# Kernel optimization log

Measured on AMD Instinct MI355X. Metric: run time of the kernel, lower is better.

## Reference

```python
import jax, jax.numpy as jnp
import numpy as np

BIT_DEPTH = 8  # feature squeezing

def setup_inputs() -> dict:
    key = jax.random.key(0)
    ks = jax.random.split(key, 8)
    B, C, H, W = 8, 256, 64, 64
    Cq = C // 8
    x = jax.random.normal(ks[0], (B, C, H, W), dtype=jnp.float32)
    # 1x1 conv weights stored as [out, in] (kernel dims squeezed)
    wq = jax.random.normal(ks[1], (Cq, C), dtype=jnp.float32) * 0.05
    bq = jax.random.normal(ks[2], (Cq,), dtype=jnp.float32) * 0.05
    wk = jax.random.normal(ks[3], (Cq, C), dtype=jnp.float32) * 0.05
    bk = jax.random.normal(ks[4], (Cq,), dtype=jnp.float32) * 0.05
    wv = jax.random.normal(ks[5], (C, C), dtype=jnp.float32) * 0.05
    bv = jax.random.normal(ks[6], (C,), dtype=jnp.float32) * 0.05
    gamma = jax.random.normal(ks[7], (1,), dtype=jnp.float32) * 0.1
    return {"x": x, "wq": wq, "bq": bq, "wk": wk, "bk": bk, "wv": wv, "bv": bv, "gamma": gamma}

def reference(x, wq, bq, wk, bk, wv, bv, gamma):
    B, C, H, W = x.shape
    N = H * W
    xf = x.reshape(B, C, N)  # flatten spatial
    # 1x1 convs == per-pixel linear projections
    q = jnp.einsum('bcn,oc->bon', xf, wq) + bq[None, :, None]   # [B, C/8, N]
    k = jnp.einsum('bcn,oc->bon', xf, wk) + bk[None, :, None]   # [B, C/8, N]
    v = jnp.einsum('bcn,oc->bon', xf, wv) + bv[None, :, None]   # [B, C, N]
    energy = jnp.einsum('bcn,bcm->bnm', q, k)                   # [B, N, N] (no scaling, as in source)
    attn = jax.nn.softmax(energy, axis=-1)
    out = jnp.einsum('bcm,bnm->bcn', v, attn).reshape(B, C, H, W)
    out = gamma[0] * out + out               # gamma-scaled residual of attention output
    scale = jnp.float32(2 ** BIT_DEPTH)
    return jnp.floor(out * scale) / scale    # feature squeezing (bit_depth=8)
```

## Files before the change

kernel.cpp:

```cpp
#include <hip/hip_runtime.h>
#include <math.h>

namespace {
constexpr int BB = 8;
constexpr int CH = 256;
constexpr int CQ = 32;
constexpr int NN = 4096;
}

typedef float f32x4 __attribute__((ext_vector_type(4)));
typedef short bf16x8 __attribute__((ext_vector_type(8)));
typedef unsigned short us8 __attribute__((ext_vector_type(8)));

#define MFMA16(a, b, c) __builtin_amdgcn_mfma_f32_16x16x32_bf16(a, b, c, 0, 0, 0)
#define LOG2E 1.4426950408889634f

__device__ __forceinline__ unsigned short f2bf(float x) {
    unsigned int u = __float_as_uint(x);
    u += 0x7fffu + ((u >> 16) & 1u);
    return (unsigned short)(u >> 16);
}
__device__ __forceinline__ float bf2f(unsigned short h) {
    return __uint_as_float(((unsigned int)h) << 16);
}
__device__ __forceinline__ void gload16(const void* g, void* l) {
    __builtin_amdgcn_global_load_lds(
        (const __attribute__((address_space(1))) unsigned int*)g,
        (__attribute__((address_space(3))) unsigned int*)l, 16, 0, 0);
}

__global__ __launch_bounds__(256) void wsplit_kernel(
    const float* __restrict__ wq, const float* __restrict__ wk,
    const float* __restrict__ wv,
    unsigned short* __restrict__ wh, unsigned short* __restrict__ wl)
{
    int idx = blockIdx.x * 256 + threadIdx.x;
    float v;
    if (idx < 8192)       v = wq[idx];
    else if (idx < 16384) v = wk[idx - 8192];
    else                  v = wv[idx - 16384];
    unsigned short hi = f2bf(v);
    wh[idx] = hi;
    wl[idx] = f2bf(v - bf2f(hi));
}

__global__ __launch_bounds__(256) void transpose_kernel(
    const float* __restrict__ x,
    unsigned short* __restrict__ xh, unsigned short* __restrict__ xl)
{
    __shared__ float xf[64 * 68];
    __shared__ unsigned short hs[64 * 80];
    __shared__ unsigned short ls[64 * 80];
    const int t  = threadIdx.x;
    const int b  = blockIdx.x >> 8;
    const int tl = blockIdx.x & 255;
    const int c0 = (tl >> 6) * 64;
    const int n0 = (tl & 63) * 64;

    #pragma unroll
    for (int i = 0; i < 4; ++i) {
        int idx = i * 256 + t;
        int c = idx >> 4, nf = idx & 15;
        float4 v4 = *(const float4*)(x + ((size_t)(b * 256 + c0 + c)) * NN + n0 + nf * 4);
        *(float4*)(xf + c * 68 + nf * 4) = v4;
    }
    __syncthreads();

    const int n = t & 63;
    #pragma unroll
    for (int loop = 0; loop < 2; ++loop) {
        int chunk = (t >> 6) + 4 * loop;
        us8 h8, l8;
        #pragma unroll
        for (int j = 0; j < 8; ++j) {
            float v = xf[(chunk * 8 + j) * 68 + n];
            unsigned short hi = f2bf(v);
            h8[j] = hi;
            l8[j] = f2bf(v - bf2f(hi));
        }
        *(us8*)(hs + n * 80 + chunk * 8) = h8;
        *(us8*)(ls + n * 80 + chunk * 8) = l8;
    }
    __syncthreads();

    {
        int rn = t >> 2, piece = t & 3;
        size_t grow = ((size_t)(b * NN + n0 + rn)) * 256 + c0 + piece * 16;
        *(us8*)(xh + grow)     = *(const us8*)(hs + rn * 80 + piece * 16);
        *(us8*)(xh + grow + 8) = *(const us8*)(hs + rn * 80 + piece * 16 + 8);
        *(us8*)(xl + grow)     = *(const us8*)(ls + rn * 80 + piece * 16);
        *(us8*)(xl + grow + 8) = *(const us8*)(ls + rn * 80 + piece * 16 + 8);
    }
}

#define PJ_XL 32768
#define PJ_VE 16384
__global__ __launch_bounds__(256, 2) void proj_kernel(
    const unsigned short* __restrict__ xh, const unsigned short* __restrict__ xl,
    const unsigned short* __restrict__ wh, const unsigned short* __restrict__ wl,
    const float* __restrict__ bq, const float* __restrict__ bk,
    const float* __restrict__ bv,
    unsigned short* __restrict__ qh, unsigned short* __restrict__ ql,
    unsigned short* __restrict__ kh, unsigned short* __restrict__ kl,
    unsigned short* __restrict__ vt)
{
    __shared__ __align__(16) unsigned char smem[65536];
    const int t    = threadIdx.x;
    const int lane = t & 63;
    const int w    = t >> 6;
    const int l16  = lane & 15;
    const int quad = lane >> 4;
    const int b    = blockIdx.x >> 6;
    const int n0   = (blockIdx.x & 63) << 6;

    const unsigned char* xhB = (const unsigned char*)(xh + ((size_t)b * NN + n0) * 256);
    const unsigned char* xlB = (const unsigned char*)(xl + ((size_t)b * NN + n0) * 256);
    #pragma unroll
    for (int j = 0; j < 8; ++j) {
        int idx = j * 256 + t;
        int r = idx >> 5, cl = idx & 31;
        int cg = cl ^ (r & 7);
        gload16(xhB + (size_t)r * 512 + cg * 16, smem + idx * 16);
        gload16(xlB + (size_t)r * 512 + cg * 16, smem + PJ_XL + idx * 16);
    }
    __syncthreads();

    f32x4 acc[5][4] = {};
    #pragma unroll 1
    for (int kc = 0; kc < 8; ++kc) {
        bf16x8 ah[5], al[5];
        #pragma unroll
        for (int i = 0; i < 5; ++i) {
            int och = (w * 5 + i) * 16 + l16;
            ah[i] = *(const bf16x8*)(wh + och * 256 + kc * 32 + quad * 8);
            al[i] = *(const bf16x8*)(wl + och * 256 + kc * 32 + quad * 8);
        }
        #pragma unroll
        for (int nt = 0; nt < 4; ++nt) {
            int roff = (nt * 16 + l16) * 512 + (((kc * 4 + quad) ^ (l16 & 7)) * 16);
            bf16x8 bh = *(const bf16x8*)(smem + roff);
            bf16x8 bl = *(const bf16x8*)(smem + PJ_XL + roff);
            #pragma unroll
            for (int i = 0; i < 5; ++i) {
                acc[i][nt] = MFMA16(ah[i], bh, acc[i][nt]);
                acc[i][nt] = MFMA16(al[i], bh, acc[i][nt]);
                acc[i][nt] = MFMA16(ah[i], bl, acc[i][nt]);
            }
        }
    }
    __syncthreads();

    #pragma unroll
    for (int i = 0; i < 5; ++i) {
        int tile = w * 5 + i;
        if (tile < 4) {
            #pragma unroll
            for (int r = 0; r < 4; ++r) {
                int och = tile * 16 + quad * 4 + r;
                float bias = (och < 32) ? bq[och] : bk[och - 32];
                int arr = (och < 32) ? 0 : 2;
                int oq = och & 31;
                #pragma unroll
                for (int nt = 0; nt < 4; ++nt) {
                    float val = acc[i][nt][r] + bias;
                    if (och < 32) val *= LOG2E;
                    unsigned short hi = f2bf(val);
                    unsigned short lo = f2bf(val - bf2f(hi));
                    *(unsigned short*)(smem + arr * 4096 + (nt * 16 + l16) * 64 + oq * 2) = hi;
                    *(unsigned short*)(smem + (arr + 1) * 4096 + (nt * 16 + l16) * 64 + oq * 2) = lo;
                }
            }
        } else {
            #pragma unroll
            for (int r = 0; r < 4; ++r) {
                int voch = tile * 16 + quad * 4 + r - 64;
                float bias = bv[voch];
                #pragma unroll
                for (int nt = 0; nt < 4; ++nt) {
                    *(unsigned short*)(smem + PJ_VE + voch * 136 + (nt * 16 + l16) * 2)
                        = f2bf(acc[i][nt][r] + bias);
                }
            }
        }
    }
    __syncthreads();

    {
        unsigned short* dsts[4] = { qh, ql, kh, kl };
        int arr = t >> 6, n = t & 63;
        unsigned short* dst = dsts[arr] + ((size_t)b * NN + n0 + n) * 32;
        #pragma unroll
        for (int i = 0; i < 4; ++i)
            *(us8*)(dst + i * 8) = *(const us8*)(smem + arr * 4096 + n * 64 + i * 16);
    }
    #pragma unroll
    for (int p = 0; p < 4; ++p) {
        int voch = p * 64 + (t >> 2), piece = t & 3;
        unsigned short* dst = vt + ((size_t)b * CH + voch) * NN + n0 + piece * 16;
        *(us8*)(dst)     = *(const us8*)(smem + PJ_VE + voch * 136 + piece * 32);
        *(us8*)(dst + 8) = *(const us8*)(smem + PJ_VE + voch * 136 + piece * 32 + 16);
    }
}

#define A_P0 0
#define A_P1 8192
#define A_V0 16384
#define A_V1 49152
#define A_SM 16384

__global__ __launch_bounds__(256, 2) void attn_kernel(
    const unsigned short* __restrict__ qh, const unsigned short* __restrict__ ql,
    const unsigned short* __restrict__ kh, const unsigned short* __restrict__ kl,
    const unsigned short* __restrict__ vt, const float* __restrict__ gptr,
    float* __restrict__ out)
{
    __shared__ __align__(16) unsigned char smem[81920];
    const int t    = threadIdx.x;
    const int lane = t & 63;
    const int w    = t >> 6;
    const int l16  = lane & 15;
    const int quad = lane >> 4;
    const int b    = blockIdx.x & 7;
    const int n0   = (blockIdx.x >> 3) << 6;

    bf16x8 qhA[4], qlA[4];
    #pragma unroll
    for (int qt = 0; qt < 4; ++qt) {
        size_t row = (size_t)b * NN + n0 + qt * 16 + l16;
        qhA[qt] = *(const bf16x8*)(qh + row * 32 + quad * 8);
        qlA[qt] = *(const bf16x8*)(ql + row * 32 + quad * 8);
    }

    const unsigned short* khbase = kh + ((size_t)b * NN + w * 16 + l16) * 32 + quad * 8;
    const unsigned short* klbase = kl + ((size_t)b * NN + w * 16 + l16) * 32 + quad * 8;
    const unsigned char*  vtB    = (const unsigned char*)(vt + (size_t)b * CH * NN);

    const unsigned char* vsrc[8];
    int vlds[8];
    #pragma unroll
    for (int j = 0; j < 8; ++j) {
        int idx = j * 256 + t;
        int r = idx >> 3, cl = idx & 7;
        int cg = cl ^ (r & 7);
        vsrc[j] = vtB + (size_t)r * 8192 + cg * 16;
        vlds[j] = idx * 16;
    }
    const int poff = l16 * 128 + ((((w << 1) | (quad >> 1)) ^ (l16 & 7)) << 4)
                   + ((quad & 1) << 3);

    f32x4 acc[4][4] = {};
    float S[4] = {};

    bf16x8 kch = *(const bf16x8*)(khbase);
    bf16x8 kcl = *(const bf16x8*)(klbase);
    #pragma unroll
    for (int j = 0; j < 8; ++j)
        gload16(vsrc[j], smem + A_V0 + vlds[j]);

    #pragma unroll 1
    for (int tile = 0; tile < 64; ++tile) {
        unsigned char* P = smem + ((tile & 1) ? A_P1 : A_P0);
        #pragma unroll
        for (int qt = 0; qt < 4; ++qt) {
            f32x4 e = { 0.f, 0.f, 0.f, 0.f };
            e = MFMA16(kch, qhA[qt], e);
            e = MFMA16(kch, qlA[qt], e);
            e = MFMA16(kcl, qhA[qt], e);
            float p0 = exp2f(e[0]), p1 = exp2f(e[1]);
            float p2 = exp2f(e[2]), p3 = exp2f(e[3]);
            unsigned int u01, u23;
            asm("v_cvt_pk_bf16_f32 %0, %1, %2" : "=v"(u01) : "v"(p0), "v"(p1));
            asm("v_cvt_pk_bf16_f32 %0, %1, %2" : "=v"(u23) : "v"(p2), "v"(p3));
            S[qt] += (__uint_as_float(u01 << 16) + __uint_as_float(u01 & 0xffff0000u))
                   + (__uint_as_float(u23 << 16) + __uint_as_float(u23 & 0xffff0000u));
            int2 pk2 = { (int)u01, (int)u23 };
            *(int2*)(P + qt * 2048 + poff) = pk2;
        }

        __syncthreads();

        const int m1 = ((tile + 1) & 63) * 64;
        bf16x8 knh = *(const bf16x8*)(khbase + (size_t)m1 * 32);
        bf16x8 knl = *(const bf16x8*)(klbase + (size_t)m1 * 32);
        if (tile < 63) {
            unsigned char* vdst = smem + ((tile & 1) ? A_V0 : A_V1);
            #pragma unroll
            for (int j = 0; j < 8; ++j) {
                vsrc[j] += 128;
                gload16(vsrc[j], vdst + vlds[j]);
            }
        }

        const unsigned char* VB = smem + ((tile & 1) ? A_V1 : A_V0);
        #pragma unroll
        for (int ks = 0; ks < 2; ++ks) {
            bf16x8 af[4], bfr[4];
            #pragma unroll
            for (int qt = 0; qt < 4; ++qt) {
                int row = qt * 16 + l16;
                af[qt] = *(const bf16x8*)(P + row * 128
                                            + (((ks * 4 + quad) ^ (l16 & 7)) << 4));
            }
            #pragma unroll
            for (int ct = 0; ct < 4; ++ct) {
                int vrow = w * 64 + ct * 16 + l16;
                bfr[ct] = *(const bf16x8*)(VB + vrow * 128
                                              + (((ks * 4 + quad) ^ (l16 & 7)) << 4));
            }
            __builtin_amdgcn_s_setprio(1);
            #pragma unroll
            for (int qt = 0; qt < 4; ++qt)
                #pragma unroll
                for (int ct = 0; ct < 4; ++ct)
                    acc[qt][ct] = MFMA16(af[qt], bfr[ct], acc[qt][ct]);
            __builtin_amdgcn_s_setprio(0);
        }
        kch = knh;
        kcl = knl;
    }

    #pragma unroll
    for (int mask = 16; mask <= 32; mask <<= 1)
        #pragma unroll
        for (int qt = 0; qt < 4; ++qt)
            S[qt] += __shfl_xor(S[qt], mask);
    float* SM = (float*)(smem + A_SM);
    if (quad == 0) {
        #pragma unroll
        for (int qt = 0; qt < 4; ++qt)
            SM[w * 64 + qt * 16 + l16] = S[qt];
    }
    __syncthreads();

    const float g1 = 1.f + gptr[0];
    float* ob = out + (size_t)b * CH * NN;
    #pragma unroll
    for (int qt = 0; qt < 4; ++qt) {
        float is[4];
        #pragma unroll
        for (int r = 0; r < 4; ++r) {
            int qi = qt * 16 + quad * 4 + r;
            float Sf = SM[qi] + SM[64 + qi] + SM[128 + qi] + SM[192 + qi];
            is[r] = g1 / Sf;
        }
        #pragma unroll
        for (int ct = 0; ct < 4; ++ct) {
            float4 o4;
            o4.x = floorf(acc[qt][ct][0] * is[0] * 256.f) * 0.00390625f;
            o4.y = floorf(acc[qt][ct][1] * is[1] * 256.f) * 0.00390625f;
            o4.z = floorf(acc[qt][ct][2] * is[2] * 256.f) * 0.00390625f;
            o4.w = floorf(acc[qt][ct][3] * is[3] * 256.f) * 0.00390625f;
            *(float4*)(ob + (size_t)(w * 64 + ct * 16 + l16) * NN
                          + n0 + qt * 16 + quad * 4) = o4;
        }
    }
}

extern "C" void kernel_launch(void* const* d_in, const int* in_sizes, int n_in,
                              void* d_out, int out_size, void* d_ws, size_t ws_size,
                              hipStream_t stream) {
    const float* x  = (const float*)d_in[0];
    const float* wq = (const float*)d_in[1];
    const float* bq = (const float*)d_in[2];
    const float* wk = (const float*)d_in[3];
    const float* bk = (const float*)d_in[4];
    const float* wv = (const float*)d_in[5];
    const float* bv = (const float*)d_in[6];
    const float* gm = (const float*)d_in[7];
    float* out = (float*)d_out;

    unsigned short* ws = (unsigned short*)d_ws;
    const size_t XSZ = (size_t)BB * NN * 256;
    const size_t WSZ = 320 * 256;
    const size_t QSZ = (size_t)BB * NN * 32;
    unsigned short* xh = ws;
    unsigned short* xl = xh + XSZ;
    unsigned short* wh = xl + XSZ;
    unsigned short* wl = wh + WSZ;
    unsigned short* qh = wl + WSZ;
    unsigned short* ql = qh + QSZ;
    unsigned short* kh = ql + QSZ;
    unsigned short* kl = kh + QSZ;
    unsigned short* vt = kl + QSZ;

    wsplit_kernel<<<320, 256, 0, stream>>>(wq, wk, wv, wh, wl);
    transpose_kernel<<<2048, 256, 0, stream>>>(x, xh, xl);
    proj_kernel<<<512, 256, 0, stream>>>(xh, xl, wh, wl, bq, bk, bv,
                                         qh, ql, kh, kl, vt);
    attn_kernel<<<512, 256, 0, stream>>>(qh, ql, kh, kl, vt, gm, out);
}
```

Baseline: 239.6 us.

## Split attention over key halves with partial outputs and combine kernel

Splits the key/value range of each query tile into two halves, so the attention stage launches twice as many blocks. Each block writes fp32 partial outputs and row sums to workspace, and a new combine kernel sums them, normalizes, and applies the quantization. The split kernel single-buffers V in shared memory with an extra barrier per tile, cutting LDS use to allow more resident blocks per CU. In exchange it adds a large fp32 round trip through global memory, an extra launch, and loses V prefetch overlap. It falls back to the original kernel if the workspace is too small.

```diff
diff --git a/kernel.cpp b/kernel.cpp
--- a/kernel.cpp
+++ b/kernel.cpp
@@ -202,26 +202,26 @@
     }
 }
 
-#define A_P0 0
-#define A_P1 8192
-#define A_V0 16384
-#define A_V1 49152
-#define A_SM 16384
-
-__global__ __launch_bounds__(256, 2) void attn_kernel(
+#define A_V  0
+#define A_P  32768
+
+__global__ __launch_bounds__(256, 4) void attn_split_kernel(
     const unsigned short* __restrict__ qh, const unsigned short* __restrict__ ql,
     const unsigned short* __restrict__ kh, const unsigned short* __restrict__ kl,
-    const unsigned short* __restrict__ vt, const float* __restrict__ gptr,
-    float* __restrict__ out)
+    const unsigned short* __restrict__ vt,
+    float* __restrict__ PO, float* __restrict__ SP)
 {
-    __shared__ __align__(16) unsigned char smem[81920];
+    __shared__ __align__(16) unsigned char smem[40960];
     const int t    = threadIdx.x;
     const int lane = t & 63;
     const int w    = t >> 6;
     const int l16  = lane & 15;
     const int quad = lane >> 4;
     const int b    = blockIdx.x & 7;
-    const int n0   = (blockIdx.x >> 3) << 6;
+    const int qi   = blockIdx.x >> 3;
+    const int qtile = qi & 63;
+    const int half  = qi >> 6;
+    const int n0   = qtile << 6;
 
     bf16x8 qhA[4], qlA[4];
     #pragma unroll
@@ -231,20 +231,22 @@
         qlA[qt] = *(const bf16x8*)(ql + row * 32 + quad * 8);
     }
 
-    const unsigned short* khbase = kh + ((size_t)b * NN + w * 16 + l16) * 32 + quad * 8;
-    const unsigned short* klbase = kl + ((size_t)b * NN + w * 16 + l16) * 32 + quad * 8;
-    const unsigned char*  vtB    = (const unsigned char*)(vt + (size_t)b * CH * NN);
-
-    const unsigned char* vsrc[8];
-    int vlds[8];
+    const unsigned short* khbase =
+        kh + ((size_t)b * NN + half * 2048 + w * 16 + l16) * 32 + quad * 8;
+    const unsigned short* klbase =
+        kl + ((size_t)b * NN + half * 2048 + w * 16 + l16) * 32 + quad * 8;
+    const unsigned char* vtB = (const unsigned char*)(vt + (size_t)b * CH * NN);
+
+    unsigned int voff[8];
     #pragma unroll
     for (int j = 0; j < 8; ++j) {
         int idx = j * 256 + t;
         int r = idx >> 3, cl = idx & 7;
         int cg = cl ^ (r & 7);
-        vsrc[j] = vtB + (size_t)r * 8192 + cg * 16;
-        vlds[j] = idx * 16;
-    }
+        voff[j] = (unsigned int)(r * 8192 + cg * 16);
+    }
+    const unsigned char* vcur = vtB + half * 4096;
+
     const int poff = l16 * 128 + ((((w << 1) | (quad >> 1)) ^ (l16 & 7)) << 4)
                    + ((quad & 1) << 3);
 
@@ -255,11 +257,11 @@
     bf16x8 kcl = *(const bf16x8*)(klbase);
     #pragma unroll
     for (int j = 0; j < 8; ++j)
-        gload16(vsrc[j], smem + A_V0 + vlds[j]);
-
+        gload16(vcur + voff[j], smem + A_V + (j * 256 + t) * 16);
+
+    unsigned char* P = smem + A_P;
     #pragma unroll 1
-    for (int tile = 0; tile < 64; ++tile) {
-        unsigned char* P = smem + ((tile & 1) ? A_P1 : A_P0);
+    for (int tile = 0; tile < 32; ++tile) {
         #pragma unroll
         for (int qt = 0; qt < 4; ++qt) {
             f32x4 e = { 0.f, 0.f, 0.f, 0.f };
@@ -279,19 +281,10 @@
 
         __syncthreads();
 
-        const int m1 = ((tile + 1) & 63) * 64;
+        const int m1 = ((tile + 1) & 31) * 64;
         bf16x8 knh = *(const bf16x8*)(khbase + (size_t)m1 * 32);
         bf16x8 knl = *(const bf16x8*)(klbase + (size_t)m1 * 32);
-        if (tile < 63) {
-            unsigned char* vdst = smem + ((tile & 1) ? A_V0 : A_V1);
-            #pragma unroll
-            for (int j = 0; j < 8; ++j) {
-                vsrc[j] += 128;
-                gload16(vsrc[j], vdst + vlds[j]);
-            }
-        }
-
-        const unsigned char* VB = smem + ((tile & 1) ? A_V1 : A_V0);
+
         #pragma unroll
         for (int ks = 0; ks < 2; ++ks) {
             bf16x8 af[4], bfr[4];
@@ -304,7 +297,7 @@
             #pragma unroll
             for (int ct = 0; ct < 4; ++ct) {
                 int vrow = w * 64 + ct * 16 + l16;
-                bfr[ct] = *(const bf16x8*)(VB + vrow * 128
+                bfr[ct] = *(const bf16x8*)(smem + A_V + vrow * 128
                                               + (((ks * 4 + quad) ^ (l16 & 7)) << 4));
             }
             __builtin_amdgcn_s_setprio(1);
@@ -315,6 +308,15 @@
                     acc[qt][ct] = MFMA16(af[qt], bfr[ct], acc[qt][ct]);
             __builtin_amdgcn_s_setprio(0);
         }
+
+        __syncthreads();
+
+        if (tile < 31) {
+            vcur += 128;
+            #pragma unroll
+            for (int j = 0; j < 8; ++j)
+                gload16(vcur + voff[j], smem + A_V + (j * 256 + t) * 16);
+        }
         kch = knh;
         kcl = knl;
     }
@@ -324,7 +326,186 @@
         #pragma unroll
         for (int qt = 0; qt < 4; ++qt)
             S[qt] += __shfl_xor(S[qt], mask);
-    float* SM = (float*)(smem + A_SM);
+    float* SM = (float*)(smem + A_P);
+    if (quad == 0) {
+        #pragma unroll
+        for (int qt = 0; qt < 4; ++qt)
+            SM[w * 64 + qt * 16 + l16] = S[qt];
+    }
+    __syncthreads();
+
+    const size_t pidx = (size_t)((half * 8 + b) * 64 + qtile);
+    if (t < 64)
+        SP[pidx * 64 + t] = SM[t] + SM[64 + t] + SM[128 + t] + SM[192 + t];
+
+    float* POb = PO + pidx * 16384;
+    #pragma unroll
+    for (int qt = 0; qt < 4; ++qt)
+        #pragma unroll
+        for (int ct = 0; ct < 4; ++ct)
+            *(f32x4*)(POb + (size_t)(w * 64 + ct * 16 + l16) * 64
+                          + qt * 16 + quad * 4) = acc[qt][ct];
+}
+
+__global__ __launch_bounds__(256) void combine_kernel(
+    const float* __restrict__ PO, const float* __restrict__ SP,
+    const float* __restrict__ gptr, float* __restrict__ out)
+{
+    const int t = threadIdx.x;
+    const int b = blockIdx.x & 7;
+    const int qtile = blockIdx.x >> 3;
+    const float g1 = 1.f + gptr[0];
+    const int q4 = t & 15, cr = t >> 4;
+
+    const size_t i0 = (size_t)((0 * 8 + b) * 64 + qtile);
+    const size_t i1 = (size_t)((1 * 8 + b) * 64 + qtile);
+    float4 s0 = *(const float4*)(SP + i0 * 64 + q4 * 4);
+    float4 s1 = *(const float4*)(SP + i1 * 64 + q4 * 4);
+    const float is0 = g1 / (s0.x + s1.x);
+    const float is1 = g1 / (s0.y + s1.y);
+    const float is2 = g1 / (s0.z + s1.z);
+    const float is3 = g1 / (s0.w + s1.w);
+
+    const float* p0 = PO + i0 * 16384;
+    const float* p1 = PO + i1 * 16384;
+    float* ob = out + (size_t)b * CH * NN + qtile * 64;
+    #pragma unroll
+    for (int cc = 0; cc < 16; ++cc) {
+        int c = cc * 16 + cr;
+        float4 a = *(const float4*)(p0 + c * 64 + q4 * 4);
+        float4 d = *(const float4*)(p1 + c * 64 + q4 * 4);
+        float4 o;
+        o.x = floorf((a.x + d.x) * is0 * 256.f) * 0.00390625f;
+        o.y = floorf((a.y + d.y) * is1 * 256.f) * 0.00390625f;
+        o.z = floorf((a.z + d.z) * is2 * 256.f) * 0.00390625f;
+        o.w = floorf((a.w + d.w) * is3 * 256.f) * 0.00390625f;
+        *(float4*)(ob + (size_t)c * NN + q4 * 4) = o;
+    }
+}
+
+#define FB_P0 0
+#define FB_P1 8192
+#define FB_V0 16384
+#define FB_V1 49152
+#define FB_SM 16384
+
+__global__ __launch_bounds__(256, 2) void attn_fb_kernel(
+    const unsigned short* __restrict__ qh, const unsigned short* __restrict__ ql,
+    const unsigned short* __restrict__ kh, const unsigned short* __restrict__ kl,
+    const unsigned short* __restrict__ vt, const float* __restrict__ gptr,
+    float* __restrict__ out)
+{
+    __shared__ __align__(16) unsigned char smem[81920];
+    const int t    = threadIdx.x;
+    const int lane = t & 63;
+    const int w    = t >> 6;
+    const int l16  = lane & 15;
+    const int quad = lane >> 4;
+    const int b    = blockIdx.x & 7;
+    const int n0   = (blockIdx.x >> 3) << 6;
+
+    bf16x8 qhA[4], qlA[4];
+    #pragma unroll
+    for (int qt = 0; qt < 4; ++qt) {
+        size_t row = (size_t)b * NN + n0 + qt * 16 + l16;
+        qhA[qt] = *(const bf16x8*)(qh + row * 32 + quad * 8);
+        qlA[qt] = *(const bf16x8*)(ql + row * 32 + quad * 8);
+    }
+
+    const unsigned short* khbase = kh + ((size_t)b * NN + w * 16 + l16) * 32 + quad * 8;
+    const unsigned short* klbase = kl + ((size_t)b * NN + w * 16 + l16) * 32 + quad * 8;
+    const unsigned char*  vtB    = (const unsigned char*)(vt + (size_t)b * CH * NN);
+
+    const unsigned char* vsrc[8];
+    int vlds[8];
+    #pragma unroll
+    for (int j = 0; j < 8; ++j) {
+        int idx = j * 256 + t;
+        int r = idx >> 3, cl = idx & 7;
+        int cg = cl ^ (r & 7);
+        vsrc[j] = vtB + (size_t)r * 8192 + cg * 16;
+        vlds[j] = idx * 16;
+    }
+    const int poff = l16 * 128 + ((((w << 1) | (quad >> 1)) ^ (l16 & 7)) << 4)
+                   + ((quad & 1) << 3);
+
+    f32x4 acc[4][4] = {};
+    float S[4] = {};
+
+    bf16x8 kch = *(const bf16x8*)(khbase);
+    bf16x8 kcl = *(const bf16x8*)(klbase);
+    #pragma unroll
+    for (int j = 0; j < 8; ++j)
+        gload16(vsrc[j], smem + FB_V0 + vlds[j]);
+
+    #pragma unroll 1
+    for (int tile = 0; tile < 64; ++tile) {
+        unsigned char* P = smem + ((tile & 1) ? FB_P1 : FB_P0);
+        #pragma unroll
+        for (int qt = 0; qt < 4; ++qt) {
+            f32x4 e = { 0.f, 0.f, 0.f, 0.f };
+            e = MFMA16(kch, qhA[qt], e);
+            e = MFMA16(kch, qlA[qt], e);
+            e = MFMA16(kcl, qhA[qt], e);
+            float p0 = exp2f(e[0]), p1 = exp2f(e[1]);
+            float p2 = exp2f(e[2]), p3 = exp2f(e[3]);
+            unsigned int u01, u23;
+            asm("v_cvt_pk_bf16_f32 %0, %1, %2" : "=v"(u01) : "v"(p0), "v"(p1));
+            asm("v_cvt_pk_bf16_f32 %0, %1, %2" : "=v"(u23) : "v"(p2), "v"(p3));
+            S[qt] += (__uint_as_float(u01 << 16) + __uint_as_float(u01 & 0xffff0000u))
+                   + (__uint_as_float(u23 << 16) + __uint_as_float(u23 & 0xffff0000u));
+            int2 pk2 = { (int)u01, (int)u23 };
+            *(int2*)(P + qt * 2048 + poff) = pk2;
+        }
+
+        __syncthreads();
+
+        const int m1 = ((tile + 1) & 63) * 64;
+        bf16x8 knh = *(const bf16x8*)(khbase + (size_t)m1 * 32);
+        bf16x8 knl = *(const bf16x8*)(klbase + (size_t)m1 * 32);
+        if (tile < 63) {
+            unsigned char* vdst = smem + ((tile & 1) ? FB_V0 : FB_V1);
+            #pragma unroll
+            for (int j = 0; j < 8; ++j) {
+                vsrc[j] += 128;
+                gload16(vsrc[j], vdst + vlds[j]);
+            }
+        }
+
+        const unsigned char* VB = smem + ((tile & 1) ? FB_V1 : FB_V0);
+        #pragma unroll
+        for (int ks = 0; ks < 2; ++ks) {
+            bf16x8 af[4], bfr[4];
+            #pragma unroll
+            for (int qt = 0; qt < 4; ++qt) {
+                int row = qt * 16 + l16;
+                af[qt] = *(const bf16x8*)(P + row * 128
+                                            + (((ks * 4 + quad) ^ (l16 & 7)) << 4));
+            }
+            #pragma unroll
+            for (int ct = 0; ct < 4; ++ct) {
+                int vrow = w * 64 + ct * 16 + l16;
+                bfr[ct] = *(const bf16x8*)(VB + vrow * 128
+                                              + (((ks * 4 + quad) ^ (l16 & 7)) << 4));
+            }
+            __builtin_amdgcn_s_setprio(1);
+            #pragma unroll
+            for (int qt = 0; qt < 4; ++qt)
+                #pragma unroll
+                for (int ct = 0; ct < 4; ++ct)
+                    acc[qt][ct] = MFMA16(af[qt], bfr[ct], acc[qt][ct]);
+            __builtin_amdgcn_s_setprio(0);
+        }
+        kch = knh;
+        kcl = knl;
+    }
+
+    #pragma unroll
+    for (int mask = 16; mask <= 32; mask <<= 1)
+        #pragma unroll
+        for (int qt = 0; qt < 4; ++qt)
+            S[qt] += __shfl_xor(S[qt], mask);
+    float* SM = (float*)(smem + FB_SM);
     if (quad == 0) {
         #pragma unroll
         for (int qt = 0; qt < 4; ++qt)
@@ -373,19 +554,31 @@
     const size_t XSZ = (size_t)BB * NN * 256;
     const size_t WSZ = 320 * 256;
     const size_t QSZ = (size_t)BB * NN * 32;
-    unsigned short* xh = ws;
-    unsigned short* xl = xh + XSZ;
-    unsigned short* wh = xl + XSZ;
-    unsigned short* wl = wh + WSZ;
-    unsigned short* qh = wl + WSZ;
+    unsigned short* qh = ws;
     unsigned short* ql = qh + QSZ;
     unsigned short* kh = ql + QSZ;
     unsigned short* kl = kh + QSZ;
     unsigned short* vt = kl + QSZ;
+    unsigned short* xh = vt + XSZ;
+    unsigned short* xl = xh + XSZ;
+    unsigned short* wh = xl + XSZ;
+    unsigned short* wl = wh + WSZ;
+
+    const size_t po_off  = (size_t)(4 * QSZ + XSZ) * 2;
+    const size_t po_sz   = (size_t)1024 * 16384 * 4;
+    const size_t sp_sz   = (size_t)1024 * 64 * 4;
+    float* PO = (float*)((char*)d_ws + po_off);
+    float* SP = (float*)((char*)d_ws + po_off + po_sz);
+    const size_t need = po_off + po_sz + sp_sz;
 
     wsplit_kernel<<<320, 256, 0, stream>>>(wq, wk, wv, wh, wl);
     transpose_kernel<<<2048, 256, 0, stream>>>(x, xh, xl);
     proj_kernel<<<512, 256, 0, stream>>>(xh, xl, wh, wl, bq, bk, bv,
                                          qh, ql, kh, kl, vt);
-    attn_kernel<<<512, 256, 0, stream>>>(qh, ql, kh, kl, vt, gm, out);
-}
+    if (ws_size >= need) {
+        attn_split_kernel<<<1024, 256, 0, stream>>>(qh, ql, kh, kl, vt, PO, SP);
+        combine_kernel<<<512, 256, 0, stream>>>(PO, SP, gm, out);
+    } else {
+        attn_fb_kernel<<<512, 256, 0, stream>>>(qh, ql, kh, kl, vt, gm, out);
+    }
+}
```

Measured after the change: 479.2 us. 2x slower.

## Single-buffer V and P tiles in LDS to double attention occupancy

Applied to the files above, without the earlier changes.

The attention kernel drops double buffering of the V tile and the P tile, cutting LDS from 80 KB to 40 KB per block and raising launch bounds from 2 to 4 blocks per CU. To make reuse of the single buffers safe, a second barrier is added after the PV MFMA loop, and the next V tile is loaded only after it. This gives up the prefetch overlap inside each block in the hope that extra resident blocks will hide the memory latency instead. The higher occupancy target may also limit registers and cause spills.

```diff
diff --git a/kernel.cpp b/kernel.cpp
--- a/kernel.cpp
+++ b/kernel.cpp
@@ -202,19 +202,16 @@
     }
 }
 
-#define A_P0 0
-#define A_P1 8192
-#define A_V0 16384
-#define A_V1 49152
-#define A_SM 16384
-
-__global__ __launch_bounds__(256, 2) void attn_kernel(
+#define A_V  0
+#define A_P  32768
+
+__global__ __launch_bounds__(256, 4) void attn_kernel(
     const unsigned short* __restrict__ qh, const unsigned short* __restrict__ ql,
     const unsigned short* __restrict__ kh, const unsigned short* __restrict__ kl,
     const unsigned short* __restrict__ vt, const float* __restrict__ gptr,
     float* __restrict__ out)
 {
-    __shared__ __align__(16) unsigned char smem[81920];
+    __shared__ __align__(16) unsigned char smem[40960];
     const int t    = threadIdx.x;
     const int lane = t & 63;
     const int w    = t >> 6;
@@ -235,16 +232,16 @@
     const unsigned short* klbase = kl + ((size_t)b * NN + w * 16 + l16) * 32 + quad * 8;
     const unsigned char*  vtB    = (const unsigned char*)(vt + (size_t)b * CH * NN);
 
-    const unsigned char* vsrc[8];
-    int vlds[8];
+    unsigned int voff[8];
     #pragma unroll
     for (int j = 0; j < 8; ++j) {
         int idx = j * 256 + t;
         int r = idx >> 3, cl = idx & 7;
         int cg = cl ^ (r & 7);
-        vsrc[j] = vtB + (size_t)r * 8192 + cg * 16;
-        vlds[j] = idx * 16;
-    }
+        voff[j] = (unsigned int)(r * 8192 + cg * 16);
+    }
+    const unsigned char* vcur = vtB;
+
     const int poff = l16 * 128 + ((((w << 1) | (quad >> 1)) ^ (l16 & 7)) << 4)
                    + ((quad & 1) << 3);
 
@@ -255,11 +252,11 @@
     bf16x8 kcl = *(const bf16x8*)(klbase);
     #pragma unroll
     for (int j = 0; j < 8; ++j)
-        gload16(vsrc[j], smem + A_V0 + vlds[j]);
-
+        gload16(vcur + voff[j], smem + A_V + (j * 256 + t) * 16);
+
+    unsigned char* P = smem + A_P;
     #pragma unroll 1
     for (int tile = 0; tile < 64; ++tile) {
-        unsigned char* P = smem + ((tile & 1) ? A_P1 : A_P0);
         #pragma unroll
         for (int qt = 0; qt < 4; ++qt) {
             f32x4 e = { 0.f, 0.f, 0.f, 0.f };
@@ -282,16 +279,7 @@
         const int m1 = ((tile + 1) & 63) * 64;
         bf16x8 knh = *(const bf16x8*)(khbase + (size_t)m1 * 32);
         bf16x8 knl = *(const bf16x8*)(klbase + (size_t)m1 * 32);
-        if (tile < 63) {
-            unsigned char* vdst = smem + ((tile & 1) ? A_V0 : A_V1);
-            #pragma unroll
-            for (int j = 0; j < 8; ++j) {
-                vsrc[j] += 128;
-                gload16(vsrc[j], vdst + vlds[j]);
-            }
-        }
-
-        const unsigned char* VB = smem + ((tile & 1) ? A_V1 : A_V0);
+
         #pragma unroll
         for (int ks = 0; ks < 2; ++ks) {
             bf16x8 af[4], bfr[4];
@@ -304,7 +292,7 @@
             #pragma unroll
             for (int ct = 0; ct < 4; ++ct) {
                 int vrow = w * 64 + ct * 16 + l16;
-                bfr[ct] = *(const bf16x8*)(VB + vrow * 128
+                bfr[ct] = *(const bf16x8*)(smem + A_V + vrow * 128
                                               + (((ks * 4 + quad) ^ (l16 & 7)) << 4));
             }
             __builtin_amdgcn_s_setprio(1);
@@ -315,6 +303,15 @@
                     acc[qt][ct] = MFMA16(af[qt], bfr[ct], acc[qt][ct]);
             __builtin_amdgcn_s_setprio(0);
         }
+
+        __syncthreads();
+
+        if (tile < 63) {
+            vcur += 128;
+            #pragma unroll
+            for (int j = 0; j < 8; ++j)
+                gload16(vcur + voff[j], smem + A_V + (j * 256 + t) * 16);
+        }
         kch = knh;
         kcl = knl;
     }
@@ -324,7 +321,7 @@
         #pragma unroll
         for (int qt = 0; qt < 4; ++qt)
             S[qt] += __shfl_xor(S[qt], mask);
-    float* SM = (float*)(smem + A_SM);
+    float* SM = (float*)(smem + A_P);
     if (quad == 0) {
         #pragma unroll
         for (int qt = 0; qt < 4; ++qt)
```

Result: slower. 547.1 us (+128.3%).
